# Kernel optimization log

Hardware: AMD Instinct MI355X
Metric: run time of the kernel (lower is better)

## Reference

```python
import jax, jax.numpy as jnp
import numpy as np

B, N, K, D, A, V = 2, 32768, 16, 256, 64, 64


def setup_inputs() -> dict:
    key = jax.random.key(0)
    ks = jax.random.split(key, 20)
    r = lambda i, shape: jax.random.normal(ks[i], shape, jnp.float32) * 0.02
    return dict(
        x=jax.random.normal(ks[0], (B, N, D), jnp.float32),
        knn_idx=jax.random.randint(ks[1], (N, K), 0, N),
        knn_rel_pos=jax.random.normal(ks[2], (N, K, 3), jnp.float32),
        g1=jnp.ones((D,), jnp.float32), b1=jnp.zeros((D,), jnp.float32),
        g2=jnp.ones((D,), jnp.float32), b2=jnp.zeros((D,), jnp.float32),
        Wq=r(3, (D, A)), bq=jnp.zeros((A,), jnp.float32),
        Wk=r(4, (D, A)), bk=jnp.zeros((A,), jnp.float32),
        Wv=r(5, (D, V)), bv=jnp.zeros((V,), jnp.float32),
        Wo=r(6, (V, D)), bo=jnp.zeros((D,), jnp.float32),
        Wpa1=r(7, (3, A)), bpa1=jnp.zeros((A,), jnp.float32),
        Wpa2=r(8, (A, A)), bpa2=jnp.zeros((A,), jnp.float32),
        Wpv1=r(9, (3, V)), bpv1=jnp.zeros((V,), jnp.float32),
        Wpv2=r(10, (V, V)), bpv2=jnp.zeros((V,), jnp.float32),
        Ws1=r(11, (A, A)), bs1=jnp.zeros((A,), jnp.float32),
        Ws2=r(12, (A, 1)), bs2=jnp.zeros((1,), jnp.float32),
        Wf1=r(13, (D, 2 * D)), bf1=jnpp if False else jnp.zeros((2 * D,), jnp.float32),
        Wf2=r(14, (2 * D, D)), bf2=jnp.zeros((D,), jnp.float32),
    )


def _ln(t, g, b):
    m = t.mean(-1, keepdims=True)
    var = ((t - m) ** 2).mean(-1, keepdims=True)
    return (t - m) * jax.lax.rsqrt(var + 1e-5) * g + b


def reference(x, knn_idx, knn_rel_pos, g1, b1, g2, b2,
              Wq, bq, Wk, bk, Wv, bv, Wo, bo,
              Wpa1, bpa1, Wpa2, bpa2, Wpv1, bpv1, Wpv2, bpv2,
              Ws1, bs1, Ws2, bs2, Wf1, bf1, Wf2, bf2):
    scale = jnp.sqrt(jnp.float32(A))
    h = _ln(x, g1, b1)                       # [B,N,D]
    q = h @ Wq + bq                          # [B,N,A]
    k_all = h @ Wk + bk                      # [B,N,A]
    v_all = h @ Wv + bv                      # [B,N,V]
    kn = k_all[:, knn_idx]                   # gather -> [B,N,K,A]
    vn = v_all[:, knn_idx]                   # [B,N,K,V]
    ra = jax.nn.relu(knn_rel_pos @ Wpa1 + bpa1) @ Wpa2 + bpa2  # [N,K,A]
    rv = jax.nn.relu(knn_rel_pos @ Wpv1 + bpv1) @ Wpv2 + bpv2  # [N,K,V]
    t = jnp.tanh(q[:, :, None, :] - kn + ra[None])             # [B,N,K,A]
    score = (jax.nn.relu(t @ Ws1 + bs1) @ Ws2 + bs2)[..., 0]   # [B,N,K]
    attn = jax.nn.softmax(score / scale, axis=2)
    ctx = jnp.einsum('bnk,bnkv->bnv', attn, vn + rv[None])     # [B,N,V]
    x = x + ctx @ Wo + bo
    h2 = _ln(x, g2, b2)
    x = x + (jax.nn.gelu(h2 @ Wf1 + bf1, approximate=False) @ Wf2 + bf2)
    return x
```

## Files before the change

kernel.cpp:

```cpp
#include <hip/hip_runtime.h>
#include <hip/hip_bf16.h>
#include <math.h>

#define BB 2
#define NN 32768
#define KK 16
#define DD 256
#define AA 64
#define VV 64

typedef __attribute__((ext_vector_type(8))) short bf16x8;
typedef __attribute__((ext_vector_type(4))) float f32x4;
typedef __attribute__((ext_vector_type(4))) unsigned short u16x4;

__device__ __forceinline__ ushort f2bf(float v) {
  __hip_bfloat16 b = __float2bfloat16(v);
  ushort u; __builtin_memcpy(&u, &b, 2);
  return u;
}
__device__ __forceinline__ float bflo(unsigned u) { return __uint_as_float(u << 16); }
__device__ __forceinline__ float bfhi(unsigned u) { return __uint_as_float(u & 0xffff0000u); }

__device__ __forceinline__ void astore(ushort* A, int row, int col, float v) {
  int off = (row * 128 + col * 2) ^ ((row & 7) << 4);
  *reinterpret_cast<ushort*>(reinterpret_cast<char*>(A) + off) = f2bf(v);
}
__device__ __forceinline__ void astore2(ushort* A, int row, int colpair, float lo, float hi) {
  int off = (row * 128 + colpair * 4) ^ ((row & 7) << 4);
  unsigned u = ((unsigned)f2bf(hi) << 16) | (unsigned)f2bf(lo);
  *reinterpret_cast<unsigned*>(reinterpret_cast<char*>(A) + off) = u;
}
__device__ __forceinline__ bf16x8 afrag(const ushort* A, int rowbase, int lane, int ks) {
  int row = rowbase + (lane & 15), g = lane >> 4;
  int off = (row * 128 + ks * 64 + g * 16) ^ ((row & 7) << 4);
  return *reinterpret_cast<const bf16x8*>(reinterpret_cast<const char*>(A) + off);
}
__device__ __forceinline__ bf16x8 loadfrag(const ushort* p, int fi, int lane) {
  return *reinterpret_cast<const bf16x8*>(&p[((size_t)fi * 64 + lane) * 8]);
}

__global__ __launch_bounds__(256) void k_prep(
    const float* __restrict__ Wq, const float* __restrict__ Wk, const float* __restrict__ Wv,
    const float* __restrict__ Wf1, const float* __restrict__ Wf2,
    const float* __restrict__ Wpa2, const float* __restrict__ Wpv2,
    const float* __restrict__ Ws1, const float* __restrict__ Wo,
    const float* __restrict__ Wpa1, const float* __restrict__ Wpv1,
    ushort* __restrict__ pQKV, ushort* __restrict__ pWf1, ushort* __restrict__ pWf2,
    ushort* __restrict__ pS, ushort* __restrict__ pWo) {
  int tid = blockIdx.x * 256 + threadIdx.x;
  int lane = tid & 63, g = lane >> 4, c16 = lane & 15;
  bf16x8 f;
  if (tid < 6144) {
    int fi = tid >> 6; int ks = fi / 12, nt = fi % 12;
    int col = nt * 16 + c16;
    const float* W = (col < 64) ? Wq : (col < 128) ? Wk : Wv;
    int c = col & 63;
#pragma unroll
    for (int e = 0; e < 8; e++) f[e] = (short)f2bf(W[(ks * 32 + g * 8 + e) * 64 + c]);
    *reinterpret_cast<bf16x8*>(&pQKV[(size_t)tid * 8]) = f;
  } else if (tid < 22528) {
    int t2 = tid - 6144; int fi = t2 >> 6; int ks = fi >> 5, nt = fi & 31;
    int col = nt * 16 + c16;
#pragma unroll
    for (int e = 0; e < 8; e++) f[e] = (short)f2bf(Wf1[(ks * 32 + g * 8 + e) * 512 + col]);
    *reinterpret_cast<bf16x8*>(&pWf1[(size_t)t2 * 8]) = f;
  } else if (tid < 38912) {
    int t3 = tid - 22528; int fi = t3 >> 6; int ks = fi >> 4, nt = fi & 15;
    int col = nt * 16 + c16;
#pragma unroll
    for (int e = 0; e < 8; e++) f[e] = (short)f2bf(Wf2[(ks * 32 + g * 8 + e) * 256 + col]);
    *reinterpret_cast<bf16x8*>(&pWf2[(size_t)t3 * 8]) = f;
  } else if (tid < 40960) {
    int t4 = tid - 38912; int fi = t4 >> 6;
    if (fi < 24) {
      int mat = fi >> 3, ks = (fi >> 2) & 1, nt = fi & 3;
      const float* W = (mat == 0) ? Wpa2 : (mat == 1) ? Wpv2 : Ws1;
      int col = nt * 16 + c16;
#pragma unroll
      for (int e = 0; e < 8; e++) f[e] = (short)f2bf(W[(ks * 32 + g * 8 + e) * 64 + col]);
    } else {
      int mat = (fi - 24) >> 2, nt = fi & 3;
      const float* W = mat ? Wpv1 : Wpa1;
      int col = nt * 16 + c16;
#pragma unroll
      for (int e = 0; e < 8; e++) {
        int K = g * 8 + e;
        f[e] = (K < 3) ? (short)f2bf(W[K * 64 + col]) : (short)0;
      }
    }
    *reinterpret_cast<bf16x8*>(&pS[(size_t)t4 * 8]) = f;
  } else if (tid < 43008) {
    int t5 = tid - 40960; int fi = t5 >> 6; int ks = fi >> 4, nt = fi & 15;
    int col = nt * 16 + c16;
#pragma unroll
    for (int e = 0; e < 8; e++) f[e] = (short)f2bf(Wo[(ks * 32 + g * 8 + e) * 256 + col]);
    *reinterpret_cast<bf16x8*>(&pWo[(size_t)t5 * 8]) = f;
  }
}

__global__ __launch_bounds__(256) void k_qkv(
    const float* __restrict__ x, const float* __restrict__ g1, const float* __restrict__ b1,
    const ushort* __restrict__ pW,
    const float* __restrict__ bq, const float* __restrict__ bk, const float* __restrict__ bv,
    ushort* __restrict__ qo, ushort* __restrict__ ko, ushort* __restrict__ vo) {
  __shared__ __align__(16) ushort hs[32 * 256];
  int t = threadIdx.x, lane = t & 63, w = t >> 6;
  size_t row0 = (size_t)blockIdx.x * 32;

  {
    const float4 gv = *reinterpret_cast<const float4*>(&g1[lane * 4]);
    const float4 bvv = *reinterpret_cast<const float4*>(&b1[lane * 4]);
#pragma unroll
    for (int r8 = 0; r8 < 8; r8++) {
      int r = w * 8 + r8;
      const float4 xv = *reinterpret_cast<const float4*>(&x[(row0 + r) * DD + lane * 4]);
      float s = xv.x + xv.y + xv.z + xv.w;
      float s2 = xv.x * xv.x + xv.y * xv.y + xv.z * xv.z + xv.w * xv.w;
      for (int o = 32; o > 0; o >>= 1) { s += __shfl_down(s, o, 64); s2 += __shfl_down(s2, o, 64); }
      s = __shfl(s, 0, 64); s2 = __shfl(s2, 0, 64);
      float m = s * (1.f / DD), rs = rsqrtf(s2 * (1.f / DD) - m * m + 1e-5f);
      u16x4 hv;
      hv[0] = f2bf((xv.x - m) * rs * gv.x + bvv.x);
      hv[1] = f2bf((xv.y - m) * rs * gv.y + bvv.y);
      hv[2] = f2bf((xv.z - m) * rs * gv.z + bvv.z);
      hv[3] = f2bf((xv.w - m) * rs * gv.w + bvv.w);
      int off = (r * 512 + lane * 8) ^ ((r & 7) << 4);
      *reinterpret_cast<u16x4*>(reinterpret_cast<char*>(hs) + off) = hv;
    }
  }
  __syncthreads();

  f32x4 acc[2][3] = {};
  bf16x8 fw[3][3];
  int rowa = lane & 15, gg = lane >> 4;
#pragma unroll
  for (int p = 0; p < 2; p++)
#pragma unroll
    for (int j = 0; j < 3; j++) fw[p][j] = loadfrag(pW, p * 12 + w * 3 + j, lane);
#pragma unroll
  for (int ks = 0; ks < 8; ks++) {
    if (ks + 2 < 8) {
#pragma unroll
      for (int j = 0; j < 3; j++) fw[(ks + 2) % 3][j] = loadfrag(pW, (ks + 2) * 12 + w * 3 + j, lane);
    }
    bf16x8 a0 = *reinterpret_cast<const bf16x8*>(reinterpret_cast<const char*>(hs) +
                 ((rowa * 512 + ks * 64 + gg * 16) ^ ((rowa & 7) << 4)));
    bf16x8 a1 = *reinterpret_cast<const bf16x8*>(reinterpret_cast<const char*>(hs) +
                 (((rowa + 16) * 512 + ks * 64 + gg * 16) ^ ((rowa & 7) << 4)));
#pragma unroll
    for (int j = 0; j < 3; j++) {
      acc[0][j] = __builtin_amdgcn_mfma_f32_16x16x32_bf16(a0, fw[ks % 3][j], acc[0][j], 0, 0, 0);
      acc[1][j] = __builtin_amdgcn_mfma_f32_16x16x32_bf16(a1, fw[ks % 3][j], acc[1][j], 0, 0, 0);
    }
  }

#pragma unroll
  for (int j = 0; j < 3; j++) {
    int ntg = w * 3 + j;
    int buf = ntg >> 2;
    ushort* out = (buf == 0) ? qo : (buf == 1) ? ko : vo;
    const float* bias = (buf == 0) ? bq : (buf == 1) ? bk : bv;
    int col = (ntg & 3) * 16 + (lane & 15);
    float bb = bias[col];
#pragma unroll
    for (int mt = 0; mt < 2; mt++)
#pragma unroll
      for (int r = 0; r < 4; r++) {
        int row = mt * 16 + (lane >> 4) * 4 + r;
        out[(row0 + row) * 64 + col] = f2bf(acc[mt][j][r] + bb);
      }
  }
}

__global__ __launch_bounds__(256) void k_attn(
    const float* __restrict__ x, const float* __restrict__ relpos, const int* __restrict__ knn,
    const ushort* __restrict__ qg, const ushort* __restrict__ kg, const ushort* __restrict__ vg,
    const float* __restrict__ bpa1, const float* __restrict__ bpa2,
    const float* __restrict__ bpv1, const float* __restrict__ bpv2,
    const ushort* __restrict__ pS, const float* __restrict__ bs1,
    const float* __restrict__ Ws2, const float* __restrict__ bs2,
    const ushort* __restrict__ pWo, const float* __restrict__ bo,
    float* __restrict__ xmid) {
  int n0 = blockIdx.x * 2;
  int t = threadIdx.x, lane = t & 63, w = t >> 6;
  int g = lane >> 4, c16 = lane & 15;
  int c2 = lane & 31, kh = lane >> 5;

  __shared__ __align__(16) ushort A0[64 * 64];
  __shared__ __align__(16) ushort ra_bs[32][72];
  __shared__ __align__(16) ushort rv_bs[32][72];
  __shared__ __align__(16) ushort hid_bs[64][72];
  __shared__ __align__(16) ushort RP[32 * 32];
  __shared__ __align__(16) ushort ctile[16 * 64];
  __shared__ __align__(8) float qv[4][64];
  __shared__ float attn_s[64];
  __shared__ int idx_s[2][16];

  if (t < 32) {
    idx_s[t >> 4][t & 15] = knn[(n0 + (t >> 4)) * KK + (t & 15)];
    float r0 = relpos[(size_t)n0 * 48 + t * 3 + 0];
    float r1 = relpos[(size_t)n0 * 48 + t * 3 + 1];
    float r2 = relpos[(size_t)n0 * 48 + t * 3 + 2];
    uint4 z; z.x = 0; z.y = 0; z.z = 0; z.w = 0;
    uint4 f0;
    f0.x = ((unsigned)f2bf(r1) << 16) | (unsigned)f2bf(r0);
    f0.y = (unsigned)f2bf(r2);
    f0.z = 0; f0.w = 0;
    *reinterpret_cast<uint4*>(&RP[t * 32 + 0])  = f0;
    *reinterpret_cast<uint4*>(&RP[t * 32 + 8])  = z;
    *reinterpret_cast<uint4*>(&RP[t * 32 + 16]) = z;
    *reinterpret_cast<uint4*>(&RP[t * 32 + 24]) = z;
  }
  qv[w][lane] = bflo(qg[((size_t)(w & 1) * NN + n0 + (w >> 1)) * AA + lane]);
  __syncthreads();

  {
    bf16x8 aRP0 = *reinterpret_cast<const bf16x8*>(&RP[(lane & 15) * 32 + g * 8]);
    bf16x8 aRP1 = *reinterpret_cast<const bf16x8*>(&RP[((lane & 15) + 16) * 32 + g * 8]);
    bf16x8 bA = loadfrag(pS, 24 + w, lane);
    bf16x8 bV = loadfrag(pS, 28 + w, lane);
    int col = w * 16 + c16;
    float ba = bpa1[col], bv1_ = bpv1[col];
    f32x4 zz = {0.f, 0.f, 0.f, 0.f};
    f32x4 hA0 = __builtin_amdgcn_mfma_f32_16x16x32_bf16(aRP0, bA, zz, 0, 0, 0);
    f32x4 hA1 = __builtin_amdgcn_mfma_f32_16x16x32_bf16(aRP1, bA, zz, 0, 0, 0);
    f32x4 hV0 = __builtin_amdgcn_mfma_f32_16x16x32_bf16(aRP0, bV, zz, 0, 0, 0);
    f32x4 hV1 = __builtin_amdgcn_mfma_f32_16x16x32_bf16(aRP1, bV, zz, 0, 0, 0);
#pragma unroll
    for (int r = 0; r < 4; r++) {
      astore(A0, 0  + g * 4 + r, col, fmaxf(hA0[r] + ba, 0.f));
      astore(A0, 16 + g * 4 + r, col, fmaxf(hA1[r] + ba, 0.f));
      astore(A0, 32 + g * 4 + r, col, fmaxf(hV0[r] + bv1_, 0.f));
      astore(A0, 48 + g * 4 + r, col, fmaxf(hV1[r] + bv1_, 0.f));
    }
  }

  unsigned kuval[8];
  {
    int pt3 = w >> 1, b3 = w & 1;
    size_t bbase = (size_t)b3 * NN;
#pragma unroll
    for (int j = 0; j < 8; j++) {
      int k = kh * 8 + j;
      kuval[j] = *reinterpret_cast<const unsigned*>(&kg[(bbase + idx_s[pt3][k]) * AA + 2 * c2]);
    }
  }
  __syncthreads();

  {
    bf16x8 bwa0 = loadfrag(pS, 0 + w, lane);
    bf16x8 bwa1 = loadfrag(pS, 4 + w, lane);
    bf16x8 bwv0 = loadfrag(pS, 8 + w, lane);
    bf16x8 bwv1 = loadfrag(pS, 12 + w, lane);
    int col = w * 16 + c16;
    float ba2 = bpa2[col], bv2 = bpv2[col];
#pragma unroll
    for (int mt = 0; mt < 2; mt++) {
      bf16x8 a0 = afrag(A0, mt * 16, lane, 0), a1 = afrag(A0, mt * 16, lane, 1);
      f32x4 acc = {0.f, 0.f, 0.f, 0.f};
      acc = __builtin_amdgcn_mfma_f32_16x16x32_bf16(a0, bwa0, acc, 0, 0, 0);
      acc = __builtin_amdgcn_mfma_f32_16x16x32_bf16(a1, bwa1, acc, 0, 0, 0);
#pragma unroll
      for (int r = 0; r < 4; r++) ra_bs[mt * 16 + g * 4 + r][col] = f2bf(acc[r] + ba2);
      bf16x8 v0 = afrag(A0, 32 + mt * 16, lane, 0), v1 = afrag(A0, 32 + mt * 16, lane, 1);
      f32x4 accv = {0.f, 0.f, 0.f, 0.f};
      accv = __builtin_amdgcn_mfma_f32_16x16x32_bf16(v0, bwv0, accv, 0, 0, 0);
      accv = __builtin_amdgcn_mfma_f32_16x16x32_bf16(v1, bwv1, accv, 0, 0, 0);
#pragma unroll
      for (int r = 0; r < 4; r++) rv_bs[mt * 16 + g * 4 + r][col] = f2bf(accv[r] + bv2);
    }
  }
  __syncthreads();

  {
    int pt = w >> 1;
    float2 qq = *reinterpret_cast<const float2*>(&qv[w][2 * c2]);
#pragma unroll
    for (int j = 0; j < 8; j++) {
      int k = kh * 8 + j;
      unsigned ku = kuval[j];
      unsigned ru = *reinterpret_cast<const unsigned*>(&ra_bs[pt * 16 + k][2 * c2]);
      float x0 = qq.x - bflo(ku) + bflo(ru);
      float x1 = qq.y - bfhi(ku) + bfhi(ru);
      float t0 = 1.f - 2.f * __builtin_amdgcn_rcpf(__expf(2.f * x0) + 1.f);
      float t1 = 1.f - 2.f * __builtin_amdgcn_rcpf(__expf(2.f * x1) + 1.f);
      astore2(A0, w * 16 + k, c2, t0, t1);
    }
  }
  __syncthreads();

  {
    bf16x8 fsA = loadfrag(pS, 16 + w, lane);
    bf16x8 fsB = loadfrag(pS, 20 + w, lane);
    int col = w * 16 + c16;
    float bsc = bs1[col], wsc = Ws2[col];
#pragma unroll
    for (int mt = 0; mt < 4; mt++) {
      bf16x8 a0 = afrag(A0, mt * 16, lane, 0), a1 = afrag(A0, mt * 16, lane, 1);
      f32x4 acc = {0.f, 0.f, 0.f, 0.f};
      acc = __builtin_amdgcn_mfma_f32_16x16x32_bf16(a0, fsA, acc, 0, 0, 0);
      acc = __builtin_amdgcn_mfma_f32_16x16x32_bf16(a1, fsB, acc, 0, 0, 0);
#pragma unroll
      for (int r = 0; r < 4; r++)
        hid_bs[mt * 16 + g * 4 + r][col] = f2bf(fmaxf(acc[r] + bsc, 0.f) * wsc);
    }
  }
  __syncthreads();

  if (t < 64) {
    const uint4* hrow = reinterpret_cast<const uint4*>(&hid_bs[t][0]);
    float s = 0.f;
#pragma unroll
    for (int c = 0; c < 8; c++) {
      uint4 v4 = hrow[c];
      s += bflo(v4.x) + bfhi(v4.x) + bflo(v4.y) + bfhi(v4.y) +
           bflo(v4.z) + bfhi(v4.z) + bflo(v4.w) + bfhi(v4.w);
    }
    float sc = (s + bs2[0]) * 0.125f;
    float mx = sc;
#pragma unroll
    for (int o = 8; o > 0; o >>= 1) mx = fmaxf(mx, __shfl_xor(mx, o, 64));
    float e = __expf(sc - mx);
    float ss = e;
#pragma unroll
    for (int o = 8; o > 0; o >>= 1) ss += __shfl_xor(ss, o, 64);
    attn_s[t] = e / ss;
  }
  __syncthreads();

  {
    int pt = w >> 1, b = w & 1;
    size_t bbase = (size_t)b * NN;
    float a0 = 0.f, a1 = 0.f;
#pragma unroll
    for (int j = 0; j < 8; j++) {
      int k = kh * 8 + j;
      const ushort* vrow = vg + (bbase + idx_s[pt][k]) * VV;
      unsigned vu = *reinterpret_cast<const unsigned*>(&vrow[2 * c2]);
      unsigned ru = *reinterpret_cast<const unsigned*>(&rv_bs[pt * 16 + k][2 * c2]);
      float aw = attn_s[w * 16 + k];
      a0 += aw * (bflo(vu) + bflo(ru));
      a1 += aw * (bfhi(vu) + bfhi(ru));
    }
    a0 += __shfl_xor(a0, 32, 64);
    a1 += __shfl_xor(a1, 32, 64);
    if (kh == 0) astore2(ctile, w, c2, a0, a1);
  }
  __syncthreads();

  {
    bf16x8 a0 = afrag(ctile, 0, lane, 0), a1 = afrag(ctile, 0, lane, 1);
    f32x4 acc[4];
#pragma unroll
    for (int j = 0; j < 4; j++) {
      bf16x8 b0 = loadfrag(pWo, 0 + w * 4 + j, lane);
      bf16x8 b1 = loadfrag(pWo, 16 + w * 4 + j, lane);
      f32x4 a = {0.f, 0.f, 0.f, 0.f};
      a = __builtin_amdgcn_mfma_f32_16x16x32_bf16(a0, b0, a, 0, 0, 0);
      a = __builtin_amdgcn_mfma_f32_16x16x32_bf16(a1, b1, a, 0, 0, 0);
      acc[j] = a;
    }
    if (g == 0) {
#pragma unroll
      for (int j = 0; j < 4; j++) {
        int col = w * 64 + j * 16 + c16;
        float bb = bo[col];
#pragma unroll
        for (int r = 0; r < 4; r++) {
          int pt = r >> 1, b = r & 1;
          size_t addr = ((size_t)b * NN + n0 + pt) * DD + col;
          xmid[addr] = x[addr] + acc[j][r] + bb;
        }
      }
    }
  }
}

__global__ __launch_bounds__(256) void k_ffn(
    const float* __restrict__ xmid, const float* __restrict__ g2, const float* __restrict__ b2,
    const ushort* __restrict__ pWf1, const float* __restrict__ bf1,
    const ushort* __restrict__ pWf2, const float* __restrict__ bf2,
    float* __restrict__ out) {
  __shared__ __align__(16) ushort hs[32 * 256];
  __shared__ __align__(16) ushort ys[32 * 512];
  int t = threadIdx.x, lane = t & 63, w = t >> 6;
  size_t row0 = (size_t)blockIdx.x * 32;
  int rowa = lane & 15, gg = lane >> 4;

  {
    const float4 gv = *reinterpret_cast<const float4*>(&g2[lane * 4]);
    const float4 bvv = *reinterpret_cast<const float4*>(&b2[lane * 4]);
#pragma unroll
    for (int r8 = 0; r8 < 8; r8++) {
      int r = w * 8 + r8;
      const float4 xv = *reinterpret_cast<const float4*>(&xmid[(row0 + r) * DD + lane * 4]);
      float s = xv.x + xv.y + xv.z + xv.w;
      float s2 = xv.x * xv.x + xv.y * xv.y + xv.z * xv.z + xv.w * xv.w;
      for (int o = 32; o > 0; o >>= 1) { s += __shfl_down(s, o, 64); s2 += __shfl_down(s2, o, 64); }
      s = __shfl(s, 0, 64); s2 = __shfl(s2, 0, 64);
      float m = s * (1.f / DD), rs = rsqrtf(s2 * (1.f / DD) - m * m + 1e-5f);
      u16x4 hv;
      hv[0] = f2bf((xv.x - m) * rs * gv.x + bvv.x);
      hv[1] = f2bf((xv.y - m) * rs * gv.y + bvv.y);
      hv[2] = f2bf((xv.z - m) * rs * gv.z + bvv.z);
      hv[3] = f2bf((xv.w - m) * rs * gv.w + bvv.w);
      int off = (r * 512 + lane * 8) ^ ((r & 7) << 4);
      *reinterpret_cast<u16x4*>(reinterpret_cast<char*>(hs) + off) = hv;
    }
  }
  __syncthreads();

  f32x4 acc1[2][8] = {};
  {
    bf16x8 fA[8], fB[8];
#pragma unroll
    for (int j = 0; j < 8; j++) fA[j] = loadfrag(pWf1, w * 8 + j, lane);
#pragma unroll
    for (int ks = 0; ks < 8; ks += 2) {
#pragma unroll
      for (int j = 0; j < 8; j++) fB[j] = loadfrag(pWf1, (ks + 1) * 32 + w * 8 + j, lane);
      {
        bf16x8 a0 = *reinterpret_cast<const bf16x8*>(reinterpret_cast<const char*>(hs) +
                     ((rowa * 512 + ks * 64 + gg * 16) ^ ((rowa & 7) << 4)));
        bf16x8 a1 = *reinterpret_cast<const bf16x8*>(reinterpret_cast<const char*>(hs) +
                     (((rowa + 16) * 512 + ks * 64 + gg * 16) ^ ((rowa & 7) << 4)));
#pragma unroll
        for (int j = 0; j < 8; j++) {
          acc1[0][j] = __builtin_amdgcn_mfma_f32_16x16x32_bf16(a0, fA[j], acc1[0][j], 0, 0, 0);
          acc1[1][j] = __builtin_amdgcn_mfma_f32_16x16x32_bf16(a1, fA[j], acc1[1][j], 0, 0, 0);
        }
      }
      if (ks + 2 < 8) {
#pragma unroll
        for (int j = 0; j < 8; j++) fA[j] = loadfrag(pWf1, (ks + 2) * 32 + w * 8 + j, lane);
      }
      {
        bf16x8 a0 = *reinterpret_cast<const bf16x8*>(reinterpret_cast<const char*>(hs) +
                     ((rowa * 512 + (ks + 1) * 64 + gg * 16) ^ ((rowa & 7) << 4)));
        bf16x8 a1 = *reinterpret_cast<const bf16x8*>(reinterpret_cast<const char*>(hs) +
                     (((rowa + 16) * 512 + (ks + 1) * 64 + gg * 16) ^ ((rowa & 7) << 4)));
#pragma unroll
        for (int j = 0; j < 8; j++) {
          acc1[0][j] = __builtin_amdgcn_mfma_f32_16x16x32_bf16(a0, fB[j], acc1[0][j], 0, 0, 0);
          acc1[1][j] = __builtin_amdgcn_mfma_f32_16x16x32_bf16(a1, fB[j], acc1[1][j], 0, 0, 0);
        }
      }
    }
  }

#pragma unroll
  for (int j = 0; j < 8; j++) {
    int col = w * 128 + j * 16 + (lane & 15);
    float bb = bf1[col];
#pragma unroll
    for (int mt = 0; mt < 2; mt++)
#pragma unroll
      for (int r = 0; r < 4; r++) {
        float v = acc1[mt][j][r] + bb;
        v = v * 0.5f * (1.f + erff(v * 0.70710678118654752f));
        int row = mt * 16 + (lane >> 4) * 4 + r;
        int off = (row * 1024 + col * 2) ^ ((row & 7) << 4);
        *reinterpret_cast<ushort*>(reinterpret_cast<char*>(ys) + off) = f2bf(v);
      }
  }
  __syncthreads();

  f32x4 acc2[2][4] = {};
  {
    bf16x8 f2[3][4];
#pragma unroll
    for (int p = 0; p < 2; p++)
#pragma unroll
      for (int j = 0; j < 4; j++) f2[p][j] = loadfrag(pWf2, p * 16 + w * 4 + j, lane);
#pragma unroll
    for (int ks = 0; ks < 16; ks++) {
      if (ks + 2 < 16) {
#pragma unroll
        for (int j = 0; j < 4; j++) f2[(ks + 2) % 3][j] = loadfrag(pWf2, (ks + 2) * 16 + w * 4 + j, lane);
      }
      bf16x8 a0 = *reinterpret_cast<const bf16x8*>(reinterpret_cast<const char*>(ys) +
                   ((rowa * 1024 + ks * 64 + gg * 16) ^ ((rowa & 7) << 4)));
      bf16x8 a1 = *reinterpret_cast<const bf16x8*>(reinterpret_cast<const char*>(ys) +
                   (((rowa + 16) * 1024 + ks * 64 + gg * 16) ^ ((rowa & 7) << 4)));
#pragma unroll
      for (int j = 0; j < 4; j++) {
        acc2[0][j] = __builtin_amdgcn_mfma_f32_16x16x32_bf16(a0, f2[ks % 3][j], acc2[0][j], 0, 0, 0);
        acc2[1][j] = __builtin_amdgcn_mfma_f32_16x16x32_bf16(a1, f2[ks % 3][j], acc2[1][j], 0, 0, 0);
      }
    }
  }

#pragma unroll
  for (int j = 0; j < 4; j++) {
    int col = w * 64 + j * 16 + (lane & 15);
    float bb = bf2[col];
#pragma unroll
    for (int mt = 0; mt < 2; mt++)
#pragma unroll
      for (int r = 0; r < 4; r++) {
        int row = mt * 16 + (lane >> 4) * 4 + r;
        size_t idx = (row0 + row) * DD + col;
        out[idx] = xmid[idx] + acc2[mt][j][r] + bb;
      }
  }
}

extern "C" void kernel_launch(void* const* d_in, const int* in_sizes, int n_in,
                              void* d_out, int out_size, void* d_ws, size_t ws_size,
                              hipStream_t stream) {
  const float* x      = (const float*)d_in[0];
  const int*   knn    = (const int*)  d_in[1];
  const float* relpos = (const float*)d_in[2];
  const float* g1     = (const float*)d_in[3];
  const float* b1     = (const float*)d_in[4];
  const float* g2     = (const float*)d_in[5];
  const float* b2     = (const float*)d_in[6];
  const float* Wq     = (const float*)d_in[7];
  const float* bq     = (const float*)d_in[8];
  const float* Wk     = (const float*)d_in[9];
  const float* bk     = (const float*)d_in[10];
  const float* Wv     = (const float*)d_in[11];
  const float* bv     = (const float*)d_in[12];
  const float* Wo     = (const float*)d_in[13];
  const float* bo     = (const float*)d_in[14];
  const float* Wpa1   = (const float*)d_in[15];
  const float* bpa1   = (const float*)d_in[16];
  const float* Wpa2   = (const float*)d_in[17];
  const float* bpa2   = (const float*)d_in[18];
  const float* Wpv1   = (const float*)d_in[19];
  const float* bpv1   = (const float*)d_in[20];
  const float* Wpv2   = (const float*)d_in[21];
  const float* bpv2   = (const float*)d_in[22];
  const float* Ws1    = (const float*)d_in[23];
  const float* bs1    = (const float*)d_in[24];
  const float* Ws2    = (const float*)d_in[25];
  const float* bs2    = (const float*)d_in[26];
  const float* Wf1    = (const float*)d_in[27];
  const float* bf1    = (const float*)d_in[28];
  const float* Wf2    = (const float*)d_in[29];
  const float* bf2    = (const float*)d_in[30];

  ushort* qb = (ushort*)d_ws;
  ushort* kb = qb + (size_t)BB * NN * AA;
  ushort* vb = kb + (size_t)BB * NN * AA;
  float* xmid = (float*)(vb + (size_t)BB * NN * VV);
  ushort* pQKV = (ushort*)(xmid + (size_t)BB * NN * DD);
  ushort* pWf1 = pQKV + 49152;
  ushort* pWf2 = pWf1 + 131072;
  ushort* pS   = pWf2 + 131072;
  ushort* pWo  = pS + 16384;

  k_prep<<<168, 256, 0, stream>>>(Wq, Wk, Wv, Wf1, Wf2, Wpa2, Wpv2, Ws1, Wo, Wpa1, Wpv1,
                                  pQKV, pWf1, pWf2, pS, pWo);
  k_qkv<<<(BB * NN) / 32, 256, 0, stream>>>(x, g1, b1, pQKV, bq, bk, bv, qb, kb, vb);
  k_attn<<<NN / 2, 256, 0, stream>>>(x, relpos, knn, qb, kb, vb,
                                     bpa1, bpa2, bpv1, bpv2,
                                     pS, bs1, Ws2, bs2, pWo, bo, xmid);
  k_ffn<<<(BB * NN) / 32, 256, 0, stream>>>(xmid, g2, b2, pWf1, bf1, pWf2, bf2, (float*)d_out);
}
```

Measured before the change: 420.1 us.

## Keep positional-encoding outputs in registers in MFMA layout, dropping shared staging

The attention kernel's thread-to-data mapping is rebuilt so each lane handles one column and the four k rows it owns in the MFMA accumulator layout. The positional-encoding outputs (ra, rv) then stay in registers instead of going through shared-memory tiles, which removes those tiles, one barrier, and the q staging buffer. The tanh input is written to a separate TT buffer. In exchange, the K and V neighbour gathers become 2-byte scalar loads per lane instead of 4-byte paired loads, and the context sum needs two cross-lane shuffles instead of one.

```diff
diff --git a/kernel.cpp b/kernel.cpp
--- a/kernel.cpp
+++ b/kernel.cpp
@@ -24,11 +24,6 @@
 __device__ __forceinline__ void astore(ushort* A, int row, int col, float v) {
   int off = (row * 128 + col * 2) ^ ((row & 7) << 4);
   *reinterpret_cast<ushort*>(reinterpret_cast<char*>(A) + off) = f2bf(v);
-}
-__device__ __forceinline__ void astore2(ushort* A, int row, int colpair, float lo, float hi) {
-  int off = (row * 128 + colpair * 4) ^ ((row & 7) << 4);
-  unsigned u = ((unsigned)f2bf(hi) << 16) | (unsigned)f2bf(lo);
-  *reinterpret_cast<unsigned*>(reinterpret_cast<char*>(A) + off) = u;
 }
 __device__ __forceinline__ bf16x8 afrag(const ushort* A, int rowbase, int lane, int ks) {
   int row = rowbase + (lane & 15), g = lane >> 4;
@@ -184,15 +179,13 @@
   int n0 = blockIdx.x * 2;
   int t = threadIdx.x, lane = t & 63, w = t >> 6;
   int g = lane >> 4, c16 = lane & 15;
-  int c2 = lane & 31, kh = lane >> 5;
+  int col = w * 16 + c16;
 
   __shared__ __align__(16) ushort A0[64 * 64];
-  __shared__ __align__(16) ushort ra_bs[32][72];
-  __shared__ __align__(16) ushort rv_bs[32][72];
+  __shared__ __align__(16) ushort TT[64 * 64];
   __shared__ __align__(16) ushort hid_bs[64][72];
   __shared__ __align__(16) ushort RP[32 * 32];
   __shared__ __align__(16) ushort ctile[16 * 64];
-  __shared__ __align__(8) float qv[4][64];
   __shared__ float attn_s[64];
   __shared__ int idx_s[2][16];
 
@@ -211,15 +204,25 @@
     *reinterpret_cast<uint4*>(&RP[t * 32 + 16]) = z;
     *reinterpret_cast<uint4*>(&RP[t * 32 + 24]) = z;
   }
-  qv[w][lane] = bflo(qg[((size_t)(w & 1) * NN + n0 + (w >> 1)) * AA + lane]);
-  __syncthreads();
+  __syncthreads();
+
+  ushort ku[2][2][4];
+  float qf[2][2];
+#pragma unroll
+  for (int pt = 0; pt < 2; pt++)
+#pragma unroll
+    for (int b = 0; b < 2; b++) {
+      qf[pt][b] = bflo((unsigned)qg[((size_t)b * NN + n0 + pt) * AA + col]);
+#pragma unroll
+      for (int r = 0; r < 4; r++)
+        ku[pt][b][r] = kg[((size_t)b * NN + idx_s[pt][g * 4 + r]) * AA + col];
+    }
 
   {
     bf16x8 aRP0 = *reinterpret_cast<const bf16x8*>(&RP[(lane & 15) * 32 + g * 8]);
     bf16x8 aRP1 = *reinterpret_cast<const bf16x8*>(&RP[((lane & 15) + 16) * 32 + g * 8]);
     bf16x8 bA = loadfrag(pS, 24 + w, lane);
     bf16x8 bV = loadfrag(pS, 28 + w, lane);
-    int col = w * 16 + c16;
     float ba = bpa1[col], bv1_ = bpv1[col];
     f32x4 zz = {0.f, 0.f, 0.f, 0.f};
     f32x4 hA0 = __builtin_amdgcn_mfma_f32_16x16x32_bf16(aRP0, bA, zz, 0, 0, 0);
@@ -234,25 +237,14 @@
       astore(A0, 48 + g * 4 + r, col, fmaxf(hV1[r] + bv1_, 0.f));
     }
   }
-
-  unsigned kuval[8];
-  {
-    int pt3 = w >> 1, b3 = w & 1;
-    size_t bbase = (size_t)b3 * NN;
-#pragma unroll
-    for (int j = 0; j < 8; j++) {
-      int k = kh * 8 + j;
-      kuval[j] = *reinterpret_cast<const unsigned*>(&kg[(bbase + idx_s[pt3][k]) * AA + 2 * c2]);
-    }
-  }
-  __syncthreads();
-
+  __syncthreads();
+
+  float ra_reg[2][4], rv_reg[2][4];
   {
     bf16x8 bwa0 = loadfrag(pS, 0 + w, lane);
     bf16x8 bwa1 = loadfrag(pS, 4 + w, lane);
     bf16x8 bwv0 = loadfrag(pS, 8 + w, lane);
     bf16x8 bwv1 = loadfrag(pS, 12 + w, lane);
-    int col = w * 16 + c16;
     float ba2 = bpa2[col], bv2 = bpv2[col];
 #pragma unroll
     for (int mt = 0; mt < 2; mt++) {
@@ -261,42 +253,36 @@
       acc = __builtin_amdgcn_mfma_f32_16x16x32_bf16(a0, bwa0, acc, 0, 0, 0);
       acc = __builtin_amdgcn_mfma_f32_16x16x32_bf16(a1, bwa1, acc, 0, 0, 0);
 #pragma unroll
-      for (int r = 0; r < 4; r++) ra_bs[mt * 16 + g * 4 + r][col] = f2bf(acc[r] + ba2);
+      for (int r = 0; r < 4; r++) ra_reg[mt][r] = acc[r] + ba2;
       bf16x8 v0 = afrag(A0, 32 + mt * 16, lane, 0), v1 = afrag(A0, 32 + mt * 16, lane, 1);
       f32x4 accv = {0.f, 0.f, 0.f, 0.f};
       accv = __builtin_amdgcn_mfma_f32_16x16x32_bf16(v0, bwv0, accv, 0, 0, 0);
       accv = __builtin_amdgcn_mfma_f32_16x16x32_bf16(v1, bwv1, accv, 0, 0, 0);
 #pragma unroll
-      for (int r = 0; r < 4; r++) rv_bs[mt * 16 + g * 4 + r][col] = f2bf(accv[r] + bv2);
-    }
-  }
-  __syncthreads();
-
-  {
-    int pt = w >> 1;
-    float2 qq = *reinterpret_cast<const float2*>(&qv[w][2 * c2]);
-#pragma unroll
-    for (int j = 0; j < 8; j++) {
-      int k = kh * 8 + j;
-      unsigned ku = kuval[j];
-      unsigned ru = *reinterpret_cast<const unsigned*>(&ra_bs[pt * 16 + k][2 * c2]);
-      float x0 = qq.x - bflo(ku) + bflo(ru);
-      float x1 = qq.y - bfhi(ku) + bfhi(ru);
-      float t0 = 1.f - 2.f * __builtin_amdgcn_rcpf(__expf(2.f * x0) + 1.f);
-      float t1 = 1.f - 2.f * __builtin_amdgcn_rcpf(__expf(2.f * x1) + 1.f);
-      astore2(A0, w * 16 + k, c2, t0, t1);
-    }
-  }
+      for (int r = 0; r < 4; r++) rv_reg[mt][r] = accv[r] + bv2;
+    }
+  }
+
+#pragma unroll
+  for (int pt = 0; pt < 2; pt++)
+#pragma unroll
+    for (int b = 0; b < 2; b++)
+#pragma unroll
+      for (int r = 0; r < 4; r++) {
+        float kf = bflo((unsigned)ku[pt][b][r]);
+        float xv = qf[pt][b] - kf + ra_reg[pt][r];
+        float tv = 1.f - 2.f * __builtin_amdgcn_rcpf(__expf(2.f * xv) + 1.f);
+        astore(TT, (pt * 2 + b) * 16 + g * 4 + r, col, tv);
+      }
   __syncthreads();
 
   {
     bf16x8 fsA = loadfrag(pS, 16 + w, lane);
     bf16x8 fsB = loadfrag(pS, 20 + w, lane);
-    int col = w * 16 + c16;
     float bsc = bs1[col], wsc = Ws2[col];
 #pragma unroll
     for (int mt = 0; mt < 4; mt++) {
-      bf16x8 a0 = afrag(A0, mt * 16, lane, 0), a1 = afrag(A0, mt * 16, lane, 1);
+      bf16x8 a0 = afrag(TT, mt * 16, lane, 0), a1 = afrag(TT, mt * 16, lane, 1);
       f32x4 acc = {0.f, 0.f, 0.f, 0.f};
       acc = __builtin_amdgcn_mfma_f32_16x16x32_bf16(a0, fsA, acc, 0, 0, 0);
       acc = __builtin_amdgcn_mfma_f32_16x16x32_bf16(a1, fsB, acc, 0, 0, 0);
@@ -329,22 +315,29 @@
   __syncthreads();
 
   {
-    int pt = w >> 1, b = w & 1;
-    size_t bbase = (size_t)b * NN;
-    float a0 = 0.f, a1 = 0.f;
-#pragma unroll
-    for (int j = 0; j < 8; j++) {
-      int k = kh * 8 + j;
-      const ushort* vrow = vg + (bbase + idx_s[pt][k]) * VV;
-      unsigned vu = *reinterpret_cast<const unsigned*>(&vrow[2 * c2]);
-      unsigned ru = *reinterpret_cast<const unsigned*>(&rv_bs[pt * 16 + k][2 * c2]);
-      float aw = attn_s[w * 16 + k];
-      a0 += aw * (bflo(vu) + bflo(ru));
-      a1 += aw * (bfhi(vu) + bfhi(ru));
-    }
-    a0 += __shfl_xor(a0, 32, 64);
-    a1 += __shfl_xor(a1, 32, 64);
-    if (kh == 0) astore2(ctile, w, c2, a0, a1);
+    float cacc[4] = {0.f, 0.f, 0.f, 0.f};
+#pragma unroll
+    for (int pt = 0; pt < 2; pt++)
+#pragma unroll
+      for (int b = 0; b < 2; b++) {
+        int mt = pt * 2 + b;
+        size_t bbase = (size_t)b * NN;
+#pragma unroll
+        for (int r = 0; r < 4; r++) {
+          int k = g * 4 + r;
+          float vf = bflo((unsigned)vg[(bbase + idx_s[pt][k]) * VV + col]);
+          cacc[mt] += attn_s[mt * 16 + k] * (vf + rv_reg[pt][r]);
+        }
+      }
+#pragma unroll
+    for (int mt = 0; mt < 4; mt++) {
+      cacc[mt] += __shfl_xor(cacc[mt], 16, 64);
+      cacc[mt] += __shfl_xor(cacc[mt], 32, 64);
+    }
+    if (g == 0) {
+#pragma unroll
+      for (int mt = 0; mt < 4; mt++) astore(ctile, mt, col, cacc[mt]);
+    }
   }
   __syncthreads();
 
@@ -363,12 +356,12 @@
     if (g == 0) {
 #pragma unroll
       for (int j = 0; j < 4; j++) {
-        int col = w * 64 + j * 16 + c16;
-        float bb = bo[col];
+        int oc = w * 64 + j * 16 + c16;
+        float bb = bo[oc];
 #pragma unroll
         for (int r = 0; r < 4; r++) {
           int pt = r >> 1, b = r & 1;
-          size_t addr = ((size_t)b * NN + n0 + pt) * DD + col;
+          size_t addr = ((size_t)b * NN + n0 + pt) * DD + oc;
           xmid[addr] = x[addr] + acc[j][r] + bb;
         }
       }
```

After: 421.7 us. About the same (+0.4%).
